# Optimization experiments

Measured on AMD Instinct MI355X. Metric: run time of the kernel, lower is better.

The kernel has to match this reference:

```python
import jax, jax.numpy as jnp
import numpy as np

L = 4        # num decoder layers
H = 8        # heads
D = 512      # d_model
DFF = 2048   # ffn hidden
V = 8000     # target vocab
B = 16       # batch
S_ENC = 128  # encoder seq len
T = 32       # decode target_length
START, END, NULL = 1, 2, 0
NEG = -1e9
EPS = 1e-6


def sinusoid_pos(max_len, d):
    pos = np.arange(max_len)[:, None].astype(np.float32)
    i = np.arange(d)[None, :].astype(np.float32)
    ang = pos / np.power(10000.0, (2.0 * np.floor(i / 2.0)) / d)
    pe = np.where(np.arange(d)[None, :] % 2 == 0, np.sin(ang), np.cos(ang))
    return jnp.asarray(pe[None], jnp.float32)  # [1, max_len, d]


def setup_inputs() -> dict:
    key = jax.random.key(0)
    ks = jax.random.split(key, 16)
    g = lambda k, shape: jax.random.normal(k, shape, jnp.float32) * 0.02
    return {
        "target_length": T,
        "encoder_output": jax.random.normal(ks[0], (B, S_ENC, D), jnp.float32),
        "padding_mask": jnp.zeros((B, S_ENC), jnp.float32),  # 1.0 where padded
        "embed": g(ks[1], (V, D)),
        "wq": g(ks[2], (L, D, D)), "wk": g(ks[3], (L, D, D)),
        "wv": g(ks[4], (L, D, D)), "wo": g(ks[5], (L, D, D)),
        "cwq": g(ks[6], (L, D, D)), "cwk": g(ks[7], (L, D, D)),
        "cwv": g(ks[8], (L, D, D)), "cwo": g(ks[9], (L, D, D)),
        "w1": g(ks[10], (L, D, DFF)), "b1": jnp.zeros((L, DFF), jnp.float32),
        "w2": g(ks[11], (L, DFF, D)), "b2": jnp.zeros((L, D), jnp.float32),
        "ln_g": jnp.ones((L, 3, D), jnp.float32), "ln_b": jnp.zeros((L, 3, D), jnp.float32),
        "fc_w": g(ks[12], (D, V)), "fc_b": jnp.zeros((V,), jnp.float32),
    }


def ln(x, g, b):
    m = jnp.mean(x, axis=-1, keepdims=True)
    v = jnp.mean(jnp.square(x - m), axis=-1, keepdims=True)
    return (x - m) * jax.lax.rsqrt(v + EPS) * g + b


def mha(q_in, kv_in, wq, wk, wv, wo, mask):
    Bn, Sq, d = q_in.shape
    dh = d // H
    q = (q_in @ wq).reshape(Bn, Sq, H, dh)
    k = (kv_in @ wk).reshape(Bn, -1, H, dh)
    v = (kv_in @ wv).reshape(Bn, -1, H, dh)
    s = jnp.einsum('bqhd,bkhd->bhqk', q, k) / jnp.sqrt(jnp.float32(dh)) + mask
    a = jax.nn.softmax(s, axis=-1)
    o = jnp.einsum('bhqk,bkhd->bqhd', a, v).reshape(Bn, Sq, d)
    return o @ wo


def decoder_stack(x, encoder_output, self_mask, cross_mask,
                  wq, wk, wv, wo, cwq, cwk, cwv, cwo,
                  w1, b1, w2, b2, ln_g, ln_b):
    for i in range(L):
        a = mha(x, x, wq[i], wk[i], wv[i], wo[i], self_mask)
        x = ln(x + a, ln_g[i, 0], ln_b[i, 0])
        a2 = mha(x, encoder_output, cwq[i], cwk[i], cwv[i], cwo[i], cross_mask)
        x = ln(x + a2, ln_g[i, 1], ln_b[i, 1])
        f = jax.nn.relu(x @ w1[i] + b1[i]) @ w2[i] + b2[i]
        x = ln(x + f, ln_g[i, 2], ln_b[i, 2])
    return x


def reference(target_length, encoder_output, padding_mask, embed,
              wq, wk, wv, wo, cwq, cwk, cwv, cwo,
              w1, b1, w2, b2, ln_g, ln_b, fc_w, fc_b):
    Bn, S, d = encoder_output.shape
    Tp1 = target_length + 1
    pos_enc = sinusoid_pos(Tp1, d)
    sqrt_d = jnp.sqrt(jnp.float32(d))
    cross_mask = padding_mask[:, None, None, :] * NEG  # [B,1,1,S_enc]
    tokens0 = jnp.full((Bn, Tp1), NULL, jnp.int32).at[:, 0].set(START)
    done0 = jnp.zeros((Bn,), bool)

    def step(carry, t):
        tokens, done = carry
        # re-embed the whole (fixed-size, masked) prefix buffer each step
        x = embed[tokens] * sqrt_d + pos_enc
        # only positions <= t are valid keys; no look-ahead mask (matches original)
        self_mask = jnp.where(jnp.arange(Tp1) <= t, 0.0, NEG)[None, None, None, :]
        x = decoder_stack(x, encoder_output, self_mask, cross_mask,
                          wq, wk, wv, wo, cwq, cwk, cwv, cwo,
                          w1, b1, w2, b2, ln_g, ln_b)
        out = x[:, t, :] @ fc_w + fc_b  # logits at last valid position
        max_idx = jnp.argmax(out, axis=-1).astype(jnp.int32)
        done = done | (max_idx == END)
        tok = jnp.where(done, jnp.int32(NULL), max_idx)
        tokens = tokens.at[:, t + 1].set(tok)
        return (tokens, done), None

    (tokens, done), _ = jax.lax.scan(step, (tokens0, done0), jnp.arange(target_length))
    return tokens[:, 1:].astype(jnp.int64)
```

## Files before the change

### kernel.cpp

```cpp
#include <hip/hip_runtime.h>
#include <math.h>

#define L_   4
#define H_   8
#define D_   512
#define DH   64
#define DFF_ 2048
#define V_   8000
#define B_   16
#define SENC 128
#define T_   32
#define TP1  33
#define NEGV -1e9f
#define EPSV 1e-6f
#define SQRTD 22.627416997969522f
#define XSZ  ((size_t)TP1 * B_ * D_)

__global__ __launch_bounds__(256) void gemm32_k(
    const float* __restrict__ A, const float* __restrict__ W,
    const float* __restrict__ bias, float* __restrict__ C,
    int M, int N, int K, int kchunk, size_t pstride, int relu, int tmode)
{
    __shared__ __align__(16) float As[2][16][34];
    __shared__ __align__(16) float Bs[2][16][68];
    int tid = threadIdx.x;
    int tx = tid & 15, ty = tid >> 4;
    int m0 = blockIdx.y * 32, n0 = blockIdx.x * 64;
    int kbeg = blockIdx.z * kchunk;
    int niter = kchunk >> 4;
    C += (size_t)blockIdx.z * pstride;
    int am = tid >> 2, aseg = tid & 3;
    int bk = tid >> 4, bc4 = (tid & 15) * 4;
    float4 aReg = make_float4(0.f, 0.f, 0.f, 0.f), bReg;
    {
        int k0 = kbeg;
        if (tid < 128) {
            int gm = m0 + am;
            if (gm < M) aReg = *(const float4*)&A[(size_t)gm * K + k0 + aseg * 4];
        }
        bReg = *(const float4*)&W[(size_t)(k0 + bk) * N + n0 + bc4];
    }
    if (tid < 128) {
        As[0][aseg * 4 + 0][am] = aReg.x;
        As[0][aseg * 4 + 1][am] = aReg.y;
        As[0][aseg * 4 + 2][am] = aReg.z;
        As[0][aseg * 4 + 3][am] = aReg.w;
    }
    *(float4*)&Bs[0][bk][bc4] = bReg;
    __syncthreads();
    float acc[2][4] = {};
    for (int it = 0; it < niter; it++) {
        int cur = it & 1;
        if (it + 1 < niter) {
            int k0 = kbeg + (it + 1) * 16;
            if (tid < 128) {
                int gm = m0 + am;
                aReg = make_float4(0.f, 0.f, 0.f, 0.f);
                if (gm < M) aReg = *(const float4*)&A[(size_t)gm * K + k0 + aseg * 4];
            }
            bReg = *(const float4*)&W[(size_t)(k0 + bk) * N + n0 + bc4];
        }
        #pragma unroll
        for (int kk = 0; kk < 16; kk++) {
            float2 a2 = *(const float2*)&As[cur][kk][ty * 2];
            float4 b4 = *(const float4*)&Bs[cur][kk][tx * 4];
            acc[0][0] += a2.x * b4.x; acc[0][1] += a2.x * b4.y;
            acc[0][2] += a2.x * b4.z; acc[0][3] += a2.x * b4.w;
            acc[1][0] += a2.y * b4.x; acc[1][1] += a2.y * b4.y;
            acc[1][2] += a2.y * b4.z; acc[1][3] += a2.y * b4.w;
        }
        if (it + 1 < niter) {
            int nxt = 1 - cur;
            if (tid < 128) {
                As[nxt][aseg * 4 + 0][am] = aReg.x;
                As[nxt][aseg * 4 + 1][am] = aReg.y;
                As[nxt][aseg * 4 + 2][am] = aReg.z;
                As[nxt][aseg * 4 + 3][am] = aReg.w;
            }
            *(float4*)&Bs[nxt][bk][bc4] = bReg;
        }
        __syncthreads();
    }
    #pragma unroll
    for (int i = 0; i < 2; i++) {
        int gm = m0 + ty * 2 + i;
        if (gm >= M) continue;
        #pragma unroll
        for (int j = 0; j < 4; j++) {
            int gn = n0 + tx * 4 + j;
            float vv = acc[i][j];
            if (bias) vv += bias[gn];
            if (relu) vv = fmaxf(vv, 0.f);
            if (tmode == 1)
                C[(size_t)(gm >> 7) * 65536 + (size_t)gn * SENC + (gm & 127)] = vv;
            else
                C[(size_t)gm * N + gn] = vv;
        }
    }
}

__global__ __launch_bounds__(256) void gemm_qkv_k(
    const float* __restrict__ A, const float* __restrict__ W0,
    const float* __restrict__ W1, const float* __restrict__ W2,
    float* __restrict__ Cb, int M)
{
    __shared__ __align__(16) float As[2][16][34];
    __shared__ __align__(16) float Bs[2][16][68];
    int sel = blockIdx.x >> 3;
    const float* W = (sel == 0) ? W0 : ((sel == 1) ? W1 : W2);
    float* C = Cb + (size_t)sel * XSZ;
    int tid = threadIdx.x;
    int tx = tid & 15, ty = tid >> 4;
    int m0 = blockIdx.y * 32, n0 = (blockIdx.x & 7) * 64;
    int am = tid >> 2, aseg = tid & 3;
    int bk = tid >> 4, bc4 = (tid & 15) * 4;
    float4 aReg = make_float4(0.f, 0.f, 0.f, 0.f), bReg;
    {
        if (tid < 128) {
            int gm = m0 + am;
            if (gm < M) aReg = *(const float4*)&A[(size_t)gm * D_ + aseg * 4];
        }
        bReg = *(const float4*)&W[(size_t)bk * D_ + n0 + bc4];
    }
    if (tid < 128) {
        As[0][aseg * 4 + 0][am] = aReg.x;
        As[0][aseg * 4 + 1][am] = aReg.y;
        As[0][aseg * 4 + 2][am] = aReg.z;
        As[0][aseg * 4 + 3][am] = aReg.w;
    }
    *(float4*)&Bs[0][bk][bc4] = bReg;
    __syncthreads();
    float acc[2][4] = {};
    for (int it = 0; it < 32; it++) {
        int cur = it & 1;
        if (it + 1 < 32) {
            int k0 = (it + 1) * 16;
            if (tid < 128) {
                int gm = m0 + am;
                aReg = make_float4(0.f, 0.f, 0.f, 0.f);
                if (gm < M) aReg = *(const float4*)&A[(size_t)gm * D_ + k0 + aseg * 4];
            }
            bReg = *(const float4*)&W[(size_t)(k0 + bk) * D_ + n0 + bc4];
        }
        #pragma unroll
        for (int kk = 0; kk < 16; kk++) {
            float2 a2 = *(const float2*)&As[cur][kk][ty * 2];
            float4 b4 = *(const float4*)&Bs[cur][kk][tx * 4];
            acc[0][0] += a2.x * b4.x; acc[0][1] += a2.x * b4.y;
            acc[0][2] += a2.x * b4.z; acc[0][3] += a2.x * b4.w;
            acc[1][0] += a2.y * b4.x; acc[1][1] += a2.y * b4.y;
            acc[1][2] += a2.y * b4.z; acc[1][3] += a2.y * b4.w;
        }
        if (it + 1 < 32) {
            int nxt = 1 - cur;
            if (tid < 128) {
                As[nxt][aseg * 4 + 0][am] = aReg.x;
                As[nxt][aseg * 4 + 1][am] = aReg.y;
                As[nxt][aseg * 4 + 2][am] = aReg.z;
                As[nxt][aseg * 4 + 3][am] = aReg.w;
            }
            *(float4*)&Bs[nxt][bk][bc4] = bReg;
        }
        __syncthreads();
    }
    #pragma unroll
    for (int i = 0; i < 2; i++) {
        int gm = m0 + ty * 2 + i;
        if (gm >= M) continue;
        #pragma unroll
        for (int j = 0; j < 4; j++) {
            int gn = n0 + tx * 4 + j;
            if (sel == 1)
                C[(size_t)(gm & 15) * 16896 + (size_t)gn * TP1 + (gm >> 4)] =
                    acc[i][j];
            else
                C[(size_t)gm * D_ + gn] = acc[i][j];
        }
    }
}

__global__ void init_k(int* __restrict__ tokens, int* __restrict__ done,
                       float* __restrict__ cmask, const float* __restrict__ pm)
{
    int tid = threadIdx.x + blockIdx.x * 256;
    if (tid < B_ * TP1) tokens[tid] = ((tid % TP1) == 0) ? 1 : 0;
    if (tid < B_) done[tid] = 0;
    if (tid < B_ * SENC) cmask[tid] = pm[tid] * NEGV;
}

__global__ __launch_bounds__(256) void embed_k(
    const float* __restrict__ embed, const int* __restrict__ tokens,
    float* __restrict__ x)
{
    int p = blockIdx.x;
    int b = blockIdx.y;
    int tok = tokens[b * TP1 + p];
    const float* e = embed + (size_t)tok * D_;
    float* xr = x + ((size_t)p * B_ + b) * D_;
    for (int d = threadIdx.x; d < D_; d += 256) {
        float fd = (float)(2 * (d / 2)) / (float)D_;
        float ang = (float)p / powf(10000.f, fd);
        float pe = (d & 1) ? cosf(ang) : sinf(ang);
        xr[d] = e[d] * SQRTD + pe;
    }
}

__device__ __forceinline__ float block_sum(float s) {
    __shared__ float red[4];
    #pragma unroll
    for (int off = 32; off; off >>= 1) s += __shfl_xor(s, off);
    if ((threadIdx.x & 63) == 0) red[threadIdx.x >> 6] = s;
    __syncthreads();
    float tot = red[0] + red[1] + red[2] + red[3];
    __syncthreads();
    return tot;
}

__global__ __launch_bounds__(256) void attn_mega_k(
    const float* __restrict__ q, const float* __restrict__ kT,
    const float* __restrict__ v, const float* __restrict__ wo,
    const float* __restrict__ KcT, const float* __restrict__ Vc,
    const float* __restrict__ cmask, const float* __restrict__ cwq,
    const float* __restrict__ cwo, float* __restrict__ x,
    const float* __restrict__ lg, const float* __restrict__ lb, int P)
{
    int r = blockIdx.x, b = r & 15;
    int tid = threadIdx.x;
    int c0 = tid * 2;
    __shared__ float xs[D_], arow[D_];
    __shared__ float scs[H_][SENC];
    __shared__ float inv[H_];
    {
        int kp = tid & 31, h = tid >> 5;
        float acc = 0.f;
        if (kp < P) {
            const float* qr = q + (size_t)r * D_ + h * 64;
            const float* kb = kT + ((size_t)(b * 8 + h) * 64) * TP1 + kp;
            #pragma unroll 8
            for (int d = 0; d < 64; d++) acc += qr[d] * kb[(size_t)d * TP1];
        }
        scs[h][kp] = acc * 0.125f;
    }
    __syncthreads();
    if (tid < 8) {
        float mx = -1e30f;
        for (int j = 0; j < P; j++) mx = fmaxf(mx, scs[tid][j]);
        float sum = 0.f;
        for (int j = 0; j < P; j++) {
            float e = expf(scs[tid][j] - mx);
            scs[tid][j] = e;
            sum += e;
        }
        inv[tid] = 1.f / sum;
    }
    __syncthreads();
    {
        int h = c0 >> 6;
        float o0 = 0.f, o1 = 0.f;
        for (int j = 0; j < P; j++) {
            float2 vv = *(const float2*)&v[((size_t)j * B_ + b) * D_ + c0];
            float w = scs[h][j];
            o0 += w * vv.x; o1 += w * vv.y;
        }
        arow[c0]     = o0 * inv[h];
        arow[c0 + 1] = o1 * inv[h];
    }
    __syncthreads();
    {
        float2 xv = *(const float2*)&x[(size_t)r * D_ + c0];
        float v0 = xv.x, v1 = xv.y;
        #pragma unroll 8
        for (int k = 0; k < D_; k++) {
            float a = arow[k];
            float2 wv = *(const float2*)&wo[(size_t)k * D_ + c0];
            v0 += a * wv.x; v1 += a * wv.y;
        }
        float mean = block_sum(v0 + v1) * (1.f / 512.f);
        float d0 = v0 - mean, d1 = v1 - mean;
        float var = block_sum(d0 * d0 + d1 * d1) * (1.f / 512.f);
        float rs = rsqrtf(var + EPSV);
        xs[c0]     = d0 * rs * lg[c0]     + lb[c0];
        xs[c0 + 1] = d1 * rs * lg[c0 + 1] + lb[c0 + 1];
    }
    __syncthreads();
    {
        float q0 = 0.f, q1 = 0.f;
        #pragma unroll 8
        for (int k = 0; k < D_; k++) {
            float a = xs[k];
            float2 wv = *(const float2*)&cwq[(size_t)k * D_ + c0];
            q0 += a * wv.x; q1 += a * wv.y;
        }
        arow[c0] = q0; arow[c0 + 1] = q1;
    }
    __syncthreads();
    #pragma unroll
    for (int j = 0; j < 4; j++) {
        int idx = tid + j * 256;
        int h = idx >> 7, s = idx & 127;
        const float* kb = KcT + ((size_t)(b * 512 + h * 64)) * SENC + s;
        float acc = 0.f;
        #pragma unroll 8
        for (int d = 0; d < 64; d++) acc += arow[h * 64 + d] * kb[(size_t)d * SENC];
        scs[h][s] = acc * 0.125f + cmask[b * SENC + s];
    }
    __syncthreads();
    if (tid < 8) {
        float mx = -1e30f;
        for (int s = 0; s < SENC; s++) mx = fmaxf(mx, scs[tid][s]);
        float sum = 0.f;
        for (int s = 0; s < SENC; s++) {
            float e = expf(scs[tid][s] - mx);
            scs[tid][s] = e;
            sum += e;
        }
        inv[tid] = 1.f / sum;
    }
    __syncthreads();
    {
        int h = c0 >> 6;
        float o0 = 0.f, o1 = 0.f;
        for (int s = 0; s < SENC; s++) {
            float2 vv = *(const float2*)&Vc[((size_t)b * SENC + s) * D_ + c0];
            float w = scs[h][s];
            o0 += w * vv.x; o1 += w * vv.y;
        }
        arow[c0]     = o0 * inv[h];
        arow[c0 + 1] = o1 * inv[h];
    }
    __syncthreads();
    {
        float v0 = xs[c0], v1 = xs[c0 + 1];
        #pragma unroll 8
        for (int k = 0; k < D_; k++) {
            float a = arow[k];
            float2 wv = *(const float2*)&cwo[(size_t)k * D_ + c0];
            v0 += a * wv.x; v1 += a * wv.y;
        }
        float mean = block_sum(v0 + v1) * (1.f / 512.f);
        float d0 = v0 - mean, d1 = v1 - mean;
        float var = block_sum(d0 * d0 + d1 * d1) * (1.f / 512.f);
        float rs = rsqrtf(var + EPSV);
        x[(size_t)r * D_ + c0]     = d0 * rs * lg[D_ + c0]     + lb[D_ + c0];
        x[(size_t)r * D_ + c0 + 1] = d1 * rs * lg[D_ + c0 + 1] + lb[D_ + c0 + 1];
    }
}

__global__ __launch_bounds__(256) void ln_red_k(
    float* __restrict__ x, const float* __restrict__ parts, size_t pstride,
    int nparts, const float* __restrict__ bias,
    const float* __restrict__ gam, const float* __restrict__ bet)
{
    int r = blockIdx.x;
    float* xr = x + (size_t)r * D_;
    int tid = threadIdx.x;
    float v0 = xr[tid];
    float v1 = xr[tid + 256];
    for (int s = 0; s < nparts; s++) {
        const float* pr = parts + (size_t)s * pstride + (size_t)r * D_;
        v0 += pr[tid];
        v1 += pr[tid + 256];
    }
    if (bias) { v0 += bias[tid]; v1 += bias[tid + 256]; }
    float mean = block_sum(v0 + v1) * (1.f / 512.f);
    float d0 = v0 - mean, d1 = v1 - mean;
    float var = block_sum(d0 * d0 + d1 * d1) * (1.f / 512.f);
    float rs = rsqrtf(var + EPSV);
    xr[tid]       = d0 * rs * gam[tid] + bet[tid];
    xr[tid + 256] = d1 * rs * gam[tid + 256] + bet[tid + 256];
}

__global__ __launch_bounds__(256) void logits_k(
    const float* __restrict__ x, const float* __restrict__ fcw,
    const float* __restrict__ fcb, float* __restrict__ cand_v,
    int* __restrict__ cand_i, int t)
{
    __shared__ float xs[B_][D_];
    __shared__ float red[4][64][B_];
    int tid = threadIdx.x;
    for (int i = tid; i < B_ * D_; i += 256) {
        int b = i >> 9, d = i & 511;
        xs[b][d] = x[((size_t)t * B_ + b) * D_ + d];
    }
    __syncthreads();
    int lane = tid & 63, ks = tid >> 6;
    int col = blockIdx.x * 64 + lane;
    float acc[B_] = {};
    int kb = ks * 128;
    for (int k = kb; k < kb + 128; k++) {
        float w = fcw[(size_t)k * V_ + col];
        #pragma unroll
        for (int b = 0; b < B_; b++) acc[b] += xs[b][k] * w;
    }
    #pragma unroll
    for (int b = 0; b < B_; b++) red[ks][lane][b] = acc[b];
    __syncthreads();
    if (ks == 0) {
        float bias = fcb[col];
        #pragma unroll
        for (int b = 0; b < B_; b++) {
            float val = red[0][lane][b] + red[1][lane][b]
                      + red[2][lane][b] + red[3][lane][b] + bias;
            int idx = col;
            #pragma unroll
            for (int off = 32; off; off >>= 1) {
                float ov = __shfl_down(val, off);
                int oi = __shfl_down(idx, off);
                if (ov > val || (ov == val && oi < idx)) { val = ov; idx = oi; }
            }
            if (lane == 0) {
                cand_v[(size_t)b * 125 + blockIdx.x] = val;
                cand_i[(size_t)b * 125 + blockIdx.x] = idx;
            }
        }
    }
}

__global__ __launch_bounds__(128) void argmax_k(
    const float* __restrict__ cand_v, const int* __restrict__ cand_i,
    int* __restrict__ tokens, int* __restrict__ done, int t)
{
    int b = blockIdx.x;
    int tid = threadIdx.x;
    float val = -1e30f; int idx = 0x7fffffff;
    if (tid < 125) { val = cand_v[(size_t)b * 125 + tid]; idx = cand_i[(size_t)b * 125 + tid]; }
    __shared__ float sv[128];
    __shared__ int si[128];
    sv[tid] = val; si[tid] = idx;
    __syncthreads();
    for (int s = 64; s; s >>= 1) {
        if (tid < s) {
            float ov = sv[tid + s]; int oi = si[tid + s];
            if (ov > sv[tid] || (ov == sv[tid] && oi < si[tid])) {
                sv[tid] = ov; si[tid] = oi;
            }
        }
        __syncthreads();
    }
    if (tid == 0) {
        int best = si[0];
        int dn = done[b] | (best == 2 ? 1 : 0);
        done[b] = dn;
        tokens[b * TP1 + t + 1] = dn ? 0 : best;
    }
}

__global__ void writeout_k(const int* __restrict__ tokens, int* __restrict__ out)
{
    int i = threadIdx.x + blockIdx.x * 256;
    if (i < B_ * T_) {
        int b = i / T_, j = i % T_;
        out[i] = tokens[b * TP1 + j + 1];
    }
}

extern "C" void kernel_launch(void* const* d_in, const int* in_sizes, int n_in,
                              void* d_out, int out_size, void* d_ws, size_t ws_size,
                              hipStream_t stream)
{
    const float* enc   = (const float*)d_in[1];
    const float* pm    = (const float*)d_in[2];
    const float* embed = (const float*)d_in[3];
    const float* wq    = (const float*)d_in[4];
    const float* wk    = (const float*)d_in[5];
    const float* wv    = (const float*)d_in[6];
    const float* wo    = (const float*)d_in[7];
    const float* cwq   = (const float*)d_in[8];
    const float* cwk   = (const float*)d_in[9];
    const float* cwv   = (const float*)d_in[10];
    const float* cwo   = (const float*)d_in[11];
    const float* w1    = (const float*)d_in[12];
    const float* b1    = (const float*)d_in[13];
    const float* w2    = (const float*)d_in[14];
    const float* b2    = (const float*)d_in[15];
    const float* ln_g  = (const float*)d_in[16];
    const float* ln_b  = (const float*)d_in[17];
    const float* fcw   = (const float*)d_in[18];
    const float* fcb   = (const float*)d_in[19];

    float* ws = (float*)d_ws;
    size_t off = 0;
    float* x     = ws + off; off += XSZ;
    float* qkv   = ws + off; off += 3 * XSZ;
    float* parts = ws + off; off += 4 * XSZ;
    float* ffnh  = ws + off; off += (size_t)TP1 * B_ * DFF_;
    float* cand_v= ws + off; off += (size_t)B_ * 125;
    float* KcT   = ws + off; off += (size_t)L_ * B_ * SENC * D_;
    float* Vc    = ws + off; off += (size_t)L_ * B_ * SENC * D_;
    float* cmask = ws + off; off += (size_t)B_ * SENC;
    int* cand_i  = (int*)(ws + off); off += (size_t)B_ * 125;
    int* tokens  = (int*)(ws + off); off += (B_ * TP1 + 63) & ~63;
    int* done    = (int*)(ws + off); off += 64;

    init_k<<<8, 256, 0, stream>>>(tokens, done, cmask, pm);

    const size_t KVL = (size_t)B_ * SENC * D_;
    for (int l = 0; l < L_; l++) {
        gemm32_k<<<dim3(8, (B_ * SENC) / 32), 256, 0, stream>>>(
            enc, cwk + (size_t)l * D_ * D_, nullptr, KcT + l * KVL,
            B_ * SENC, D_, D_, D_, 0, 0, 1);
        gemm32_k<<<dim3(8, (B_ * SENC) / 32), 256, 0, stream>>>(
            enc, cwv + (size_t)l * D_ * D_, nullptr, Vc + l * KVL,
            B_ * SENC, D_, D_, D_, 0, 0, 0);
    }

    for (int t = 0; t < T_; t++) {
        int P = t + 1;
        int M = P * B_;
        int mt = (M + 31) / 32;

        embed_k<<<dim3(P, B_), 256, 0, stream>>>(embed, tokens, x);

        for (int l = 0; l < L_; l++) {
            const size_t lw = (size_t)l * D_ * D_;
            gemm_qkv_k<<<dim3(24, mt), 256, 0, stream>>>(
                x, wq + lw, wk + lw, wv + lw, qkv, M);
            attn_mega_k<<<M, 256, 0, stream>>>(
                qkv, qkv + XSZ, qkv + 2 * XSZ, wo + lw,
                KcT + l * KVL, Vc + l * KVL, cmask, cwq + lw, cwo + lw, x,
                ln_g + (size_t)(l * 3 + 0) * D_, ln_b + (size_t)(l * 3 + 0) * D_, P);
            gemm32_k<<<dim3(32, mt), 256, 0, stream>>>(
                x, w1 + (size_t)l * D_ * DFF_, b1 + (size_t)l * DFF_, ffnh,
                M, DFF_, D_, D_, 0, 1, 0);
            gemm32_k<<<dim3(8, mt, 4), 256, 0, stream>>>(
                ffnh, w2 + (size_t)l * DFF_ * D_, nullptr, parts,
                M, D_, DFF_, 512, XSZ, 0, 0);
            ln_red_k<<<M, 256, 0, stream>>>(x, parts, XSZ, 4, b2 + (size_t)l * D_,
                ln_g + (size_t)(l * 3 + 2) * D_, ln_b + (size_t)(l * 3 + 2) * D_);
        }

        logits_k<<<V_ / 64, 256, 0, stream>>>(x, fcw, fcb, cand_v, cand_i, t);
        argmax_k<<<B_, 128, 0, stream>>>(cand_v, cand_i, tokens, done, t);
    }

    writeout_k<<<2, 256, 0, stream>>>(tokens, (int*)d_out);
}
```

Baseline: 24.40 ms.

## Enlarge GEMM tiles, pre-transpose attention weights, fuse argmax into embed

The GEMM kernels move from 32x64 to 64x64 tiles, with 4x4 register blocking per thread and float4 stores, so each block reuses more of every loaded weight. The wo, cwq and cwo weights are transposed once into workspace, which lets the per-row matvecs in the attention kernel read contiguous float4 rows instead of strided columns. Positional encodings are precomputed once per call, and the argmax step is folded into the next step's embed kernel and into the final writeout, removing one launch per decode step. In exchange it needs extra workspace, and with fewer M tiles the small early decode steps launch fewer blocks.

```diff
diff --git a/kernel.cpp b/kernel.cpp
--- a/kernel.cpp
+++ b/kernel.cpp
@@ -15,17 +15,18 @@
 #define EPSV 1e-6f
 #define SQRTD 22.627416997969522f
 #define XSZ  ((size_t)TP1 * B_ * D_)
+#define DD   ((size_t)D_ * D_)
 
 __global__ __launch_bounds__(256) void gemm32_k(
     const float* __restrict__ A, const float* __restrict__ W,
     const float* __restrict__ bias, float* __restrict__ C,
     int M, int N, int K, int kchunk, size_t pstride, int relu, int tmode)
 {
-    __shared__ __align__(16) float As[2][16][34];
+    __shared__ __align__(16) float As[2][16][68];
     __shared__ __align__(16) float Bs[2][16][68];
     int tid = threadIdx.x;
     int tx = tid & 15, ty = tid >> 4;
-    int m0 = blockIdx.y * 32, n0 = blockIdx.x * 64;
+    int m0 = blockIdx.y * 64, n0 = blockIdx.x * 64;
     int kbeg = blockIdx.z * kchunk;
     int niter = kchunk >> 4;
     C += (size_t)blockIdx.z * pstride;
@@ -33,68 +34,75 @@
     int bk = tid >> 4, bc4 = (tid & 15) * 4;
     float4 aReg = make_float4(0.f, 0.f, 0.f, 0.f), bReg;
     {
-        int k0 = kbeg;
-        if (tid < 128) {
-            int gm = m0 + am;
-            if (gm < M) aReg = *(const float4*)&A[(size_t)gm * K + k0 + aseg * 4];
-        }
-        bReg = *(const float4*)&W[(size_t)(k0 + bk) * N + n0 + bc4];
-    }
-    if (tid < 128) {
-        As[0][aseg * 4 + 0][am] = aReg.x;
-        As[0][aseg * 4 + 1][am] = aReg.y;
-        As[0][aseg * 4 + 2][am] = aReg.z;
-        As[0][aseg * 4 + 3][am] = aReg.w;
-    }
+        int gm = m0 + am;
+        if (gm < M) aReg = *(const float4*)&A[(size_t)gm * K + kbeg + aseg * 4];
+        bReg = *(const float4*)&W[(size_t)(kbeg + bk) * N + n0 + bc4];
+    }
+    As[0][aseg * 4 + 0][am] = aReg.x;
+    As[0][aseg * 4 + 1][am] = aReg.y;
+    As[0][aseg * 4 + 2][am] = aReg.z;
+    As[0][aseg * 4 + 3][am] = aReg.w;
     *(float4*)&Bs[0][bk][bc4] = bReg;
     __syncthreads();
-    float acc[2][4] = {};
+    float acc[4][4] = {};
     for (int it = 0; it < niter; it++) {
         int cur = it & 1;
         if (it + 1 < niter) {
             int k0 = kbeg + (it + 1) * 16;
-            if (tid < 128) {
-                int gm = m0 + am;
-                aReg = make_float4(0.f, 0.f, 0.f, 0.f);
-                if (gm < M) aReg = *(const float4*)&A[(size_t)gm * K + k0 + aseg * 4];
-            }
+            int gm = m0 + am;
+            aReg = make_float4(0.f, 0.f, 0.f, 0.f);
+            if (gm < M) aReg = *(const float4*)&A[(size_t)gm * K + k0 + aseg * 4];
             bReg = *(const float4*)&W[(size_t)(k0 + bk) * N + n0 + bc4];
         }
         #pragma unroll
         for (int kk = 0; kk < 16; kk++) {
-            float2 a2 = *(const float2*)&As[cur][kk][ty * 2];
+            float4 a4 = *(const float4*)&As[cur][kk][ty * 4];
             float4 b4 = *(const float4*)&Bs[cur][kk][tx * 4];
-            acc[0][0] += a2.x * b4.x; acc[0][1] += a2.x * b4.y;
-            acc[0][2] += a2.x * b4.z; acc[0][3] += a2.x * b4.w;
-            acc[1][0] += a2.y * b4.x; acc[1][1] += a2.y * b4.y;
-            acc[1][2] += a2.y * b4.z; acc[1][3] += a2.y * b4.w;
+            acc[0][0] += a4.x * b4.x; acc[0][1] += a4.x * b4.y;
+            acc[0][2] += a4.x * b4.z; acc[0][3] += a4.x * b4.w;
+            acc[1][0] += a4.y * b4.x; acc[1][1] += a4.y * b4.y;
+            acc[1][2] += a4.y * b4.z; acc[1][3] += a4.y * b4.w;
+            acc[2][0] += a4.z * b4.x; acc[2][1] += a4.z * b4.y;
+            acc[2][2] += a4.z * b4.z; acc[2][3] += a4.z * b4.w;
+            acc[3][0] += a4.w * b4.x; acc[3][1] += a4.w * b4.y;
+            acc[3][2] += a4.w * b4.z; acc[3][3] += a4.w * b4.w;
         }
         if (it + 1 < niter) {
             int nxt = 1 - cur;
-            if (tid < 128) {
-                As[nxt][aseg * 4 + 0][am] = aReg.x;
-                As[nxt][aseg * 4 + 1][am] = aReg.y;
-                As[nxt][aseg * 4 + 2][am] = aReg.z;
-                As[nxt][aseg * 4 + 3][am] = aReg.w;
-            }
+            As[nxt][aseg * 4 + 0][am] = aReg.x;
+            As[nxt][aseg * 4 + 1][am] = aReg.y;
+            As[nxt][aseg * 4 + 2][am] = aReg.z;
+            As[nxt][aseg * 4 + 3][am] = aReg.w;
             *(float4*)&Bs[nxt][bk][bc4] = bReg;
         }
         __syncthreads();
     }
     #pragma unroll
-    for (int i = 0; i < 2; i++) {
-        int gm = m0 + ty * 2 + i;
+    for (int i = 0; i < 4; i++) {
+        int gm = m0 + ty * 4 + i;
         if (gm >= M) continue;
-        #pragma unroll
-        for (int j = 0; j < 4; j++) {
-            int gn = n0 + tx * 4 + j;
-            float vv = acc[i][j];
-            if (bias) vv += bias[gn];
-            if (relu) vv = fmaxf(vv, 0.f);
-            if (tmode == 1)
+        if (tmode == 1) {
+            #pragma unroll
+            for (int j = 0; j < 4; j++) {
+                int gn = n0 + tx * 4 + j;
+                float vv = acc[i][j];
+                if (bias) vv += bias[gn];
+                if (relu) vv = fmaxf(vv, 0.f);
                 C[(size_t)(gm >> 7) * 65536 + (size_t)gn * SENC + (gm & 127)] = vv;
-            else
-                C[(size_t)gm * N + gn] = vv;
+            }
+        } else {
+            int gn = n0 + tx * 4;
+            float4 o;
+            o.x = acc[i][0]; o.y = acc[i][1]; o.z = acc[i][2]; o.w = acc[i][3];
+            if (bias) {
+                o.x += bias[gn + 0]; o.y += bias[gn + 1];
+                o.z += bias[gn + 2]; o.w += bias[gn + 3];
+            }
+            if (relu) {
+                o.x = fmaxf(o.x, 0.f); o.y = fmaxf(o.y, 0.f);
+                o.z = fmaxf(o.z, 0.f); o.w = fmaxf(o.w, 0.f);
+            }
+            *(float4*)&C[(size_t)gm * N + gn] = o;
         }
     }
 }
@@ -104,77 +112,76 @@
     const float* __restrict__ W1, const float* __restrict__ W2,
     float* __restrict__ Cb, int M)
 {
-    __shared__ __align__(16) float As[2][16][34];
+    __shared__ __align__(16) float As[2][16][68];
     __shared__ __align__(16) float Bs[2][16][68];
     int sel = blockIdx.x >> 3;
     const float* W = (sel == 0) ? W0 : ((sel == 1) ? W1 : W2);
     float* C = Cb + (size_t)sel * XSZ;
     int tid = threadIdx.x;
     int tx = tid & 15, ty = tid >> 4;
-    int m0 = blockIdx.y * 32, n0 = (blockIdx.x & 7) * 64;
+    int m0 = blockIdx.y * 64, n0 = (blockIdx.x & 7) * 64;
     int am = tid >> 2, aseg = tid & 3;
     int bk = tid >> 4, bc4 = (tid & 15) * 4;
     float4 aReg = make_float4(0.f, 0.f, 0.f, 0.f), bReg;
     {
-        if (tid < 128) {
-            int gm = m0 + am;
-            if (gm < M) aReg = *(const float4*)&A[(size_t)gm * D_ + aseg * 4];
-        }
+        int gm = m0 + am;
+        if (gm < M) aReg = *(const float4*)&A[(size_t)gm * D_ + aseg * 4];
         bReg = *(const float4*)&W[(size_t)bk * D_ + n0 + bc4];
     }
-    if (tid < 128) {
-        As[0][aseg * 4 + 0][am] = aReg.x;
-        As[0][aseg * 4 + 1][am] = aReg.y;
-        As[0][aseg * 4 + 2][am] = aReg.z;
-        As[0][aseg * 4 + 3][am] = aReg.w;
-    }
+    As[0][aseg * 4 + 0][am] = aReg.x;
+    As[0][aseg * 4 + 1][am] = aReg.y;
+    As[0][aseg * 4 + 2][am] = aReg.z;
+    As[0][aseg * 4 + 3][am] = aReg.w;
     *(float4*)&Bs[0][bk][bc4] = bReg;
     __syncthreads();
-    float acc[2][4] = {};
+    float acc[4][4] = {};
     for (int it = 0; it < 32; it++) {
         int cur = it & 1;
         if (it + 1 < 32) {
             int k0 = (it + 1) * 16;
-            if (tid < 128) {
-                int gm = m0 + am;
-                aReg = make_float4(0.f, 0.f, 0.f, 0.f);
-                if (gm < M) aReg = *(const float4*)&A[(size_t)gm * D_ + k0 + aseg * 4];
-            }
+            int gm = m0 + am;
+            aReg = make_float4(0.f, 0.f, 0.f, 0.f);
+            if (gm < M) aReg = *(const float4*)&A[(size_t)gm * D_ + k0 + aseg * 4];
             bReg = *(const float4*)&W[(size_t)(k0 + bk) * D_ + n0 + bc4];
         }
         #pragma unroll
         for (int kk = 0; kk < 16; kk++) {
-            float2 a2 = *(const float2*)&As[cur][kk][ty * 2];
+            float4 a4 = *(const float4*)&As[cur][kk][ty * 4];
             float4 b4 = *(const float4*)&Bs[cur][kk][tx * 4];
-            acc[0][0] += a2.x * b4.x; acc[0][1] += a2.x * b4.y;
-            acc[0][2] += a2.x * b4.z; acc[0][3] += a2.x * b4.w;
-            acc[1][0] += a2.y * b4.x; acc[1][1] += a2.y * b4.y;
-            acc[1][2] += a2.y * b4.z; acc[1][3] += a2.y * b4.w;
+            acc[0][0] += a4.x * b4.x; acc[0][1] += a4.x * b4.y;
+            acc[0][2] += a4.x * b4.z; acc[0][3] += a4.x * b4.w;
+            acc[1][0] += a4.y * b4.x; acc[1][1] += a4.y * b4.y;
+            acc[1][2] += a4.y * b4.z; acc[1][3] += a4.y * b4.w;
+            acc[2][0] += a4.z * b4.x; acc[2][1] += a4.z * b4.y;
+            acc[2][2] += a4.z * b4.z; acc[2][3] += a4.z * b4.w;
+            acc[3][0] += a4.w * b4.x; acc[3][1] += a4.w * b4.y;
+            acc[3][2] += a4.w * b4.z; acc[3][3] += a4.w * b4.w;
         }
         if (it + 1 < 32) {
             int nxt = 1 - cur;
-            if (tid < 128) {
-                As[nxt][aseg * 4 + 0][am] = aReg.x;
-                As[nxt][aseg * 4 + 1][am] = aReg.y;
-                As[nxt][aseg * 4 + 2][am] = aReg.z;
-                As[nxt][aseg * 4 + 3][am] = aReg.w;
-            }
+            As[nxt][aseg * 4 + 0][am] = aReg.x;
+            As[nxt][aseg * 4 + 1][am] = aReg.y;
+            As[nxt][aseg * 4 + 2][am] = aReg.z;
+            As[nxt][aseg * 4 + 3][am] = aReg.w;
             *(float4*)&Bs[nxt][bk][bc4] = bReg;
         }
         __syncthreads();
     }
     #pragma unroll
-    for (int i = 0; i < 2; i++) {
-        int gm = m0 + ty * 2 + i;
+    for (int i = 0; i < 4; i++) {
+        int gm = m0 + ty * 4 + i;
         if (gm >= M) continue;
-        #pragma unroll
-        for (int j = 0; j < 4; j++) {
-            int gn = n0 + tx * 4 + j;
-            if (sel == 1)
+        if (sel == 1) {
+            #pragma unroll
+            for (int j = 0; j < 4; j++) {
+                int gn = n0 + tx * 4 + j;
                 C[(size_t)(gm & 15) * 16896 + (size_t)gn * TP1 + (gm >> 4)] =
                     acc[i][j];
-            else
-                C[(size_t)gm * D_ + gn] = acc[i][j];
+            }
+        } else {
+            float4 o;
+            o.x = acc[i][0]; o.y = acc[i][1]; o.z = acc[i][2]; o.w = acc[i][3];
+            *(float4*)&C[(size_t)gm * D_ + n0 + tx * 4] = o;
         }
     }
 }
@@ -188,21 +195,89 @@
     if (tid < B_ * SENC) cmask[tid] = pm[tid] * NEGV;
 }
 
-__global__ __launch_bounds__(256) void embed_k(
-    const float* __restrict__ embed, const int* __restrict__ tokens,
-    float* __restrict__ x)
+__global__ __launch_bounds__(256) void pe_k(float* __restrict__ pe)
 {
     int p = blockIdx.x;
-    int b = blockIdx.y;
-    int tok = tokens[b * TP1 + p];
-    const float* e = embed + (size_t)tok * D_;
-    float* xr = x + ((size_t)p * B_ + b) * D_;
     for (int d = threadIdx.x; d < D_; d += 256) {
         float fd = (float)(2 * (d / 2)) / (float)D_;
         float ang = (float)p / powf(10000.f, fd);
-        float pe = (d & 1) ? cosf(ang) : sinf(ang);
-        xr[d] = e[d] * SQRTD + pe;
-    }
+        pe[(size_t)p * D_ + d] = (d & 1) ? cosf(ang) : sinf(ang);
+    }
+}
+
+__global__ __launch_bounds__(256) void transpose_k(
+    const float* __restrict__ wo, const float* __restrict__ cwq,
+    const float* __restrict__ cwo, float* __restrict__ dst)
+{
+    __shared__ float tile[32][33];
+    int z = blockIdx.z;
+    int sel = z >> 2, l = z & 3;
+    const float* src = (sel == 0) ? wo : ((sel == 1) ? cwq : cwo);
+    src += (size_t)l * DD;
+    float* d = dst + (size_t)z * DD;
+    int x0 = blockIdx.x * 32, y0 = blockIdx.y * 32;
+    int lx = threadIdx.x & 31, ly = threadIdx.x >> 5;
+    #pragma unroll
+    for (int r = 0; r < 32; r += 8)
+        tile[ly + r][lx] = src[(size_t)(y0 + ly + r) * D_ + x0 + lx];
+    __syncthreads();
+    #pragma unroll
+    for (int r = 0; r < 32; r += 8)
+        d[(size_t)(x0 + ly + r) * D_ + y0 + lx] = tile[lx][ly + r];
+}
+
+__global__ __launch_bounds__(256) void embed_k(
+    const float* __restrict__ embed, int* __restrict__ tokens,
+    float* __restrict__ x, const float* __restrict__ pe,
+    const float* __restrict__ cand_v, const int* __restrict__ cand_i,
+    int* __restrict__ done, int t)
+{
+    int p = blockIdx.x;
+    int b = blockIdx.y;
+    int tid = threadIdx.x;
+    __shared__ float sv[128];
+    __shared__ int si[128];
+    __shared__ int stok;
+    if (p == t && t > 0) {
+        if (tid < 128) {
+            float val = -1e30f; int idx = 0x7fffffff;
+            if (tid < 125) {
+                val = cand_v[(size_t)b * 125 + tid];
+                idx = cand_i[(size_t)b * 125 + tid];
+            }
+            sv[tid] = val; si[tid] = idx;
+        }
+        __syncthreads();
+        for (int s = 64; s; s >>= 1) {
+            if (tid < s) {
+                float ov = sv[tid + s]; int oi = si[tid + s];
+                if (ov > sv[tid] || (ov == sv[tid] && oi < si[tid])) {
+                    sv[tid] = ov; si[tid] = oi;
+                }
+            }
+            __syncthreads();
+        }
+        if (tid == 0) {
+            int best = si[0];
+            int dn = done[b] | (best == 2 ? 1 : 0);
+            done[b] = dn;
+            int tk = dn ? 0 : best;
+            tokens[b * TP1 + t] = tk;
+            stok = tk;
+        }
+        __syncthreads();
+    }
+    int tok = (p == t && t > 0) ? stok : tokens[b * TP1 + p];
+    const float* e = embed + (size_t)tok * D_;
+    const float* pr = pe + (size_t)p * D_;
+    float* xr = x + ((size_t)p * B_ + b) * D_;
+    int c0 = tid * 2;
+    float2 ev = *(const float2*)&e[c0];
+    float2 pv = *(const float2*)&pr[c0];
+    float2 o;
+    o.x = ev.x * SQRTD + pv.x;
+    o.y = ev.y * SQRTD + pv.y;
+    *(float2*)&xr[c0] = o;
 }
 
 __device__ __forceinline__ float block_sum(float s) {
@@ -222,7 +297,7 @@
     const float* __restrict__ KcT, const float* __restrict__ Vc,
     const float* __restrict__ cmask, const float* __restrict__ cwq,
     const float* __restrict__ cwo, float* __restrict__ x,
-    const float* __restrict__ lg, const float* __restrict__ lb, int P)
+    const float* __restrict__ lg, const float* __restrict__ lb, int P, int wt)
 {
     int r = blockIdx.x, b = r & 15;
     int tid = threadIdx.x;
@@ -269,11 +344,25 @@
     {
         float2 xv = *(const float2*)&x[(size_t)r * D_ + c0];
         float v0 = xv.x, v1 = xv.y;
-        #pragma unroll 8
-        for (int k = 0; k < D_; k++) {
-            float a = arow[k];
-            float2 wv = *(const float2*)&wo[(size_t)k * D_ + c0];
-            v0 += a * wv.x; v1 += a * wv.y;
+        if (wt) {
+            const float* wr0 = wo + (size_t)c0 * D_;
+            const float* wr1 = wr0 + D_;
+            #pragma unroll 8
+            for (int k = 0; k < D_; k += 4) {
+                float4 wa = *(const float4*)&wr0[k];
+                float4 wb = *(const float4*)&wr1[k];
+                float a0 = arow[k], a1 = arow[k + 1];
+                float a2 = arow[k + 2], a3 = arow[k + 3];
+                v0 += a0 * wa.x; v0 += a1 * wa.y; v0 += a2 * wa.z; v0 += a3 * wa.w;
+                v1 += a0 * wb.x; v1 += a1 * wb.y; v1 += a2 * wb.z; v1 += a3 * wb.w;
+            }
+        } else {
+            #pragma unroll 8
+            for (int k = 0; k < D_; k++) {
+                float a = arow[k];
+                float2 wv = *(const float2*)&wo[(size_t)k * D_ + c0];
+                v0 += a * wv.x; v1 += a * wv.y;
+            }
         }
         float mean = block_sum(v0 + v1) * (1.f / 512.f);
         float d0 = v0 - mean, d1 = v1 - mean;
@@ -285,11 +374,25 @@
     __syncthreads();
     {
         float q0 = 0.f, q1 = 0.f;
-        #pragma unroll 8
-        for (int k = 0; k < D_; k++) {
-            float a = xs[k];
-            float2 wv = *(const float2*)&cwq[(size_t)k * D_ + c0];
-            q0 += a * wv.x; q1 += a * wv.y;
+        if (wt) {
+            const float* wr0 = cwq + (size_t)c0 * D_;
+            const float* wr1 = wr0 + D_;
+            #pragma unroll 8
+            for (int k = 0; k < D_; k += 4) {
+                float4 wa = *(const float4*)&wr0[k];
+                float4 wb = *(const float4*)&wr1[k];
+                float a0 = xs[k], a1 = xs[k + 1];
+                float a2 = xs[k + 2], a3 = xs[k + 3];
+                q0 += a0 * wa.x; q0 += a1 * wa.y; q0 += a2 * wa.z; q0 += a3 * wa.w;
+                q1 += a0 * wb.x; q1 += a1 * wb.y; q1 += a2 * wb.z; q1 += a3 * wb.w;
+            }
+        } else {
+            #pragma unroll 8
+            for (int k = 0; k < D_; k++) {
+                float a = xs[k];
+                float2 wv = *(const float2*)&cwq[(size_t)k * D_ + c0];
+                q0 += a * wv.x; q1 += a * wv.y;
+            }
         }
         arow[c0] = q0; arow[c0 + 1] = q1;
     }
@@ -331,11 +434,25 @@
     __syncthreads();
     {
         float v0 = xs[c0], v1 = xs[c0 + 1];
-        #pragma unroll 8
-        for (int k = 0; k < D_; k++) {
-            float a = arow[k];
-            float2 wv = *(const float2*)&cwo[(size_t)k * D_ + c0];
-            v0 += a * wv.x; v1 += a * wv.y;
+        if (wt) {
+            const float* wr0 = cwo + (size_t)c0 * D_;
+            const float* wr1 = wr0 + D_;
+            #pragma unroll 8
+            for (int k = 0; k < D_; k += 4) {
+                float4 wa = *(const float4*)&wr0[k];
+                float4 wb = *(const float4*)&wr1[k];
+                float a0 = arow[k], a1 = arow[k + 1];
+                float a2 = arow[k + 2], a3 = arow[k + 3];
+                v0 += a0 * wa.x; v0 += a1 * wa.y; v0 += a2 * wa.z; v0 += a3 * wa.w;
+                v1 += a0 * wb.x; v1 += a1 * wb.y; v1 += a2 * wb.z; v1 += a3 * wb.w;
+            }
+        } else {
+            #pragma unroll 8
+            for (int k = 0; k < D_; k++) {
+                float a = arow[k];
+                float2 wv = *(const float2*)&cwo[(size_t)k * D_ + c0];
+                v0 += a * wv.x; v1 += a * wv.y;
+            }
         }
         float mean = block_sum(v0 + v1) * (1.f / 512.f);
         float d0 = v0 - mean, d1 = v1 - mean;
@@ -416,16 +533,21 @@
     }
 }
 
-__global__ __launch_bounds__(128) void argmax_k(
-    const float* __restrict__ cand_v, const int* __restrict__ cand_i,
-    int* __restrict__ tokens, int* __restrict__ done, int t)
+__global__ __launch_bounds__(128) void writeout_k(
+    const int* __restrict__ tokens, const float* __restrict__ cand_v,
+    const int* __restrict__ cand_i, const int* __restrict__ done,
+    int* __restrict__ out)
 {
     int b = blockIdx.x;
     int tid = threadIdx.x;
-    float val = -1e30f; int idx = 0x7fffffff;
-    if (tid < 125) { val = cand_v[(size_t)b * 125 + tid]; idx = cand_i[(size_t)b * 125 + tid]; }
     __shared__ float sv[128];
     __shared__ int si[128];
+    __shared__ int stok;
+    float val = -1e30f; int idx = 0x7fffffff;
+    if (tid < 125) {
+        val = cand_v[(size_t)b * 125 + tid];
+        idx = cand_i[(size_t)b * 125 + tid];
+    }
     sv[tid] = val; si[tid] = idx;
     __syncthreads();
     for (int s = 64; s; s >>= 1) {
@@ -440,18 +562,11 @@
     if (tid == 0) {
         int best = si[0];
         int dn = done[b] | (best == 2 ? 1 : 0);
-        done[b] = dn;
-        tokens[b * TP1 + t + 1] = dn ? 0 : best;
-    }
-}
-
-__global__ void writeout_k(const int* __restrict__ tokens, int* __restrict__ out)
-{
-    int i = threadIdx.x + blockIdx.x * 256;
-    if (i < B_ * T_) {
-        int b = i / T_, j = i % T_;
-        out[i] = tokens[b * TP1 + j + 1];
-    }
+        stok = dn ? 0 : best;
+    }
+    __syncthreads();
+    if (tid < T_)
+        out[b * T_ + tid] = (tid == T_ - 1) ? stok : tokens[b * TP1 + tid + 1];
 }
 
 extern "C" void kernel_launch(void* const* d_in, const int* in_sizes, int n_in,
@@ -488,18 +603,24 @@
     float* KcT   = ws + off; off += (size_t)L_ * B_ * SENC * D_;
     float* Vc    = ws + off; off += (size_t)L_ * B_ * SENC * D_;
     float* cmask = ws + off; off += (size_t)B_ * SENC;
+    float* pe    = ws + off; off += (size_t)TP1 * D_;
     int* cand_i  = (int*)(ws + off); off += (size_t)B_ * 125;
     int* tokens  = (int*)(ws + off); off += (B_ * TP1 + 63) & ~63;
     int* done    = (int*)(ws + off); off += 64;
+    float* wT    = ws + off; off += 12 * DD;
+    int wtflag = (ws_size >= off * sizeof(float)) ? 1 : 0;
 
     init_k<<<8, 256, 0, stream>>>(tokens, done, cmask, pm);
+    pe_k<<<TP1, 256, 0, stream>>>(pe);
+    if (wtflag)
+        transpose_k<<<dim3(16, 16, 12), 256, 0, stream>>>(wo, cwq, cwo, wT);
 
     const size_t KVL = (size_t)B_ * SENC * D_;
     for (int l = 0; l < L_; l++) {
-        gemm32_k<<<dim3(8, (B_ * SENC) / 32), 256, 0, stream>>>(
+        gemm32_k<<<dim3(8, (B_ * SENC) / 64), 256, 0, stream>>>(
             enc, cwk + (size_t)l * D_ * D_, nullptr, KcT + l * KVL,
             B_ * SENC, D_, D_, D_, 0, 0, 1);
-        gemm32_k<<<dim3(8, (B_ * SENC) / 32), 256, 0, stream>>>(
+        gemm32_k<<<dim3(8, (B_ * SENC) / 64), 256, 0, stream>>>(
             enc, cwv + (size_t)l * D_ * D_, nullptr, Vc + l * KVL,
             B_ * SENC, D_, D_, D_, 0, 0, 0);
     }
@@ -507,18 +628,23 @@
     for (int t = 0; t < T_; t++) {
         int P = t + 1;
         int M = P * B_;
-        int mt = (M + 31) / 32;
-
-        embed_k<<<dim3(P, B_), 256, 0, stream>>>(embed, tokens, x);
+        int mt = (M + 63) / 64;
+
+        embed_k<<<dim3(P, B_), 256, 0, stream>>>(
+            embed, tokens, x, pe, cand_v, cand_i, done, t);
 
         for (int l = 0; l < L_; l++) {
             const size_t lw = (size_t)l * D_ * D_;
+            const float* woP  = wtflag ? wT + (size_t)(0 + l) * DD : wo + lw;
+            const float* cwqP = wtflag ? wT + (size_t)(4 + l) * DD : cwq + lw;
+            const float* cwoP = wtflag ? wT + (size_t)(8 + l) * DD : cwo + lw;
             gemm_qkv_k<<<dim3(24, mt), 256, 0, stream>>>(
                 x, wq + lw, wk + lw, wv + lw, qkv, M);
             attn_mega_k<<<M, 256, 0, stream>>>(
-                qkv, qkv + XSZ, qkv + 2 * XSZ, wo + lw,
-                KcT + l * KVL, Vc + l * KVL, cmask, cwq + lw, cwo + lw, x,
-                ln_g + (size_t)(l * 3 + 0) * D_, ln_b + (size_t)(l * 3 + 0) * D_, P);
+                qkv, qkv + XSZ, qkv + 2 * XSZ, woP,
+                KcT + l * KVL, Vc + l * KVL, cmask, cwqP, cwoP, x,
+                ln_g + (size_t)(l * 3 + 0) * D_, ln_b + (size_t)(l * 3 + 0) * D_,
+                P, wtflag);
             gemm32_k<<<dim3(32, mt), 256, 0, stream>>>(
                 x, w1 + (size_t)l * D_ * DFF_, b1 + (size_t)l * DFF_, ffnh,
                 M, DFF_, D_, D_, 0, 1, 0);
@@ -530,8 +656,7 @@
         }
 
         logits_k<<<V_ / 64, 256, 0, stream>>>(x, fcw, fcb, cand_v, cand_i, t);
-        argmax_k<<<B_, 128, 0, stream>>>(cand_v, cand_i, tokens, done, t);
-    }
-
-    writeout_k<<<2, 256, 0, stream>>>(tokens, (int*)d_out);
-}
+    }
+
+    writeout_k<<<B_, 128, 0, stream>>>(tokens, cand_v, cand_i, done, (int*)d_out);
+}
```

Result: slower. 32.01 ms (+31.2%).
